# Performance work log

Hardware: AMD Instinct MI355X
Metric: run time of the kernel (lower is better)

Reference implementation:

```python
import jax, jax.numpy as jnp
import numpy as np

E = 64          # num experts
IN = 512        # input_size
OUT = 512       # output_size
N = 131072      # total tokens = sum(expert_size)
CAP = 3072      # static per-expert capacity (>= max expert_size)


def _make_expert_sizes():
    # uneven but deterministic sizes summing to N, all <= CAP
    rng = np.random.default_rng(0)
    sizes = np.full(E, N // E, dtype=np.int32)
    d = rng.integers(0, 513, size=E // 2).astype(np.int32)
    sizes[0::2] += d
    sizes[1::2] -= d
    assert sizes.sum() == N and sizes.max() <= CAP and sizes.min() > 0
    return jnp.asarray(sizes, dtype=jnp.int32)


def setup_inputs() -> dict:
    key = jax.random.key(0)
    k1, k2 = jax.random.split(key)
    inputs = jax.random.normal(k1, (N, IN), dtype=jnp.float32)
    # matches nn.init.uniform_(weight, -1/in, 1/in)
    weight = jax.random.uniform(k2, (E, IN, OUT), dtype=jnp.float32,
                                minval=-1.0 / IN, maxval=1.0 / IN)
    expert_size = _make_expert_sizes()
    return {"inputs": inputs, "expert_size": expert_size, "weight": weight}


def reference(inputs, expert_size, weight):
    # Grouped GEMM: tokens are pre-sorted by expert; segment e is
    # inputs[offset[e]:offset[e]+expert_size[e]] @ weight[e].
    cap_ids = jnp.arange(CAP, dtype=jnp.int32)                # [CAP]
    offsets = jnp.cumsum(expert_size) - expert_size           # [E]
    idx = offsets[:, None] + cap_ids[None, :]                 # [E, CAP]
    valid = cap_ids[None, :] < expert_size[:, None]           # [E, CAP]
    idx = jnp.where(valid, idx, N)                            # invalid -> OOB (dropped)
    # gather tokens into padded per-expert blocks; invalid slots -> 0
    x = jnp.take(inputs, idx, axis=0, mode='fill', fill_value=0.0)  # [E, CAP, IN]
    h = jnp.einsum('eci,eio->eco', x, weight)                 # [E, CAP, OUT]
    out = jnp.zeros((N, OUT), dtype=inputs.dtype)
    out = out.at[idx.reshape(-1)].add(h.reshape(-1, OUT), mode='drop')
    return out
```

## Files before the change

kernel.cpp:

```cpp
#include <hip/hip_runtime.h>
#include <hip/hip_bf16.h>

#define E_NUM 64
#define IN_SZ 512
#define OUT_SZ 512
#define N_TOK 131072
#define CAP 3072

#define BM 128
#define BN 256
#define BK 32
#define THREADS 512
#define RT_MAX 24
#define CT_NUM 2
#define JT 16
#define NWG (E_NUM * RT_MAX * CT_NUM)

typedef __attribute__((ext_vector_type(8))) short short8;
typedef __attribute__((ext_vector_type(4))) float f32x4;

__device__ inline unsigned short f2bf(float f) {
    unsigned int u = __float_as_uint(f);
    unsigned int r = (u + 0x7FFF + ((u >> 16) & 1)) >> 16;
    return (unsigned short)r;
}

#define GLOAD_LDS16(g, l)                                                     \
    __builtin_amdgcn_global_load_lds(                                         \
        (const __attribute__((address_space(1))) void*)(g),                   \
        (__attribute__((address_space(3))) void*)(l), 16, 0, 0)

__global__ void offsets_kernel(const int* __restrict__ sizes, int* __restrict__ offs) {
    int e = threadIdx.x;
    int s = 0;
    for (int i = 0; i < e; ++i) s += sizes[i];
    offs[e] = s;
}

__global__ __launch_bounds__(256) void prep_wt(const float* __restrict__ W,
                                               unsigned short* __restrict__ WT) {
    __shared__ float t[32][33];
    int k0 = blockIdx.x * 32, n0 = blockIdx.y * 32, e = blockIdx.z;
    const float* We = W + (size_t)e * IN_SZ * OUT_SZ;
    int tid = threadIdx.x;
    int r = tid >> 3, c4 = (tid & 7) * 4;
    float4 v = *(const float4*)(We + (size_t)(k0 + r) * OUT_SZ + n0 + c4);
    t[r][c4 + 0] = v.x; t[r][c4 + 1] = v.y; t[r][c4 + 2] = v.z; t[r][c4 + 3] = v.w;
    __syncthreads();
    ushort4 o;
    o.x = f2bf(t[c4 + 0][r]);
    o.y = f2bf(t[c4 + 1][r]);
    o.z = f2bf(t[c4 + 2][r]);
    o.w = f2bf(t[c4 + 3][r]);
    unsigned short* O = WT + (size_t)e * IN_SZ * OUT_SZ + (size_t)(n0 + r) * IN_SZ + k0 + c4;
    *(ushort4*)O = o;
}

__global__ __launch_bounds__(THREADS, 4) void gemm_moe(
    const float* __restrict__ A, const int* __restrict__ sizes,
    const unsigned short* __restrict__ WT, const int* __restrict__ offs,
    float* __restrict__ out)
{
    int b0 = blockIdx.x;
    int wg = (b0 & 7) * (NWG / 8) + (b0 >> 3);
    int ct = wg & (CT_NUM - 1);
    int rt = (wg >> 1) % RT_MAX;
    int e  = wg / (RT_MAX * CT_NUM);

    int size_e = sizes[e];
    int rows0 = rt * BM;
    if (rows0 >= size_e) return;
    int off_e = offs[e];
    int rows_rem = size_e - rows0;
    int maxr = (rows_rem < BM ? rows_rem : BM) - 1;

    __shared__ unsigned short lsA[2][BM * BK];
    __shared__ unsigned short lsB[2][BN * BK];

    int tid = threadIdx.x, l = tid & 63, w = tid >> 6;
    const char* WTe = (const char*)(WT + (size_t)e * IN_SZ * OUT_SZ);
    const float* Abase = A + (size_t)(off_e + rows0) * IN_SZ;

    const float* ap[2];
    int aw[2];
    #pragma unroll
    for (int i = 0; i < 2; ++i) {
        int idx = tid + THREADS * i;
        int row = idx >> 3, c4 = idx & 7;
        int gr = row <= maxr ? row : maxr;
        ap[i] = Abase + (size_t)gr * IN_SZ + c4 * 4;
        aw[i] = row * 64 + ((c4 * 8) ^ (((row >> 1) & 3) << 4));
    }
    const char* gB[2];
    #pragma unroll
    for (int i = 0; i < 2; ++i) {
        int c = w * 2 + i;
        int n = c * 16 + (l >> 2);
        int csrc = ((l & 3) * 16) ^ (((l >> 3) & 3) << 4);
        gB[i] = WTe + (size_t)(ct * BN + n) * (IN_SZ * 2) + csrc;
    }

    float4 ar[2];

    auto loadA = [&](int kt) {
        #pragma unroll
        for (int i = 0; i < 2; ++i)
            ar[i] = *(const float4*)(ap[i] + kt * BK);
    };
    auto writeA = [&](int buf) {
        #pragma unroll
        for (int i = 0; i < 2; ++i) {
            ushort4 pk;
            pk.x = f2bf(ar[i].x); pk.y = f2bf(ar[i].y);
            pk.z = f2bf(ar[i].z); pk.w = f2bf(ar[i].w);
            *(ushort4*)((char*)&lsA[buf][0] + aw[i]) = pk;
        }
    };
    auto stageB = [&](int buf, int kt) {
        #pragma unroll
        for (int i = 0; i < 2; ++i)
            GLOAD_LDS16(gB[i] + kt * 64, &lsB[buf][(w * 2 + i) * 512]);
    };

    int wm = (w >> 2) * 64, wn = (w & 3) * 64;
    int lrow = l & 15;
    int cb = ((l >> 4) * 16) ^ (((l >> 1) & 3) << 4);

    f32x4 acc[4][4] = {};

    loadA(0); stageB(0, 0);
    writeA(0);
    __syncthreads();

    #pragma unroll
    for (int j = 0; j < JT; ++j) {
        int cur = j & 1;
        if (j + 1 < JT) {
            loadA(j + 1);
            stageB(cur ^ 1, j + 1);
        }
        {
            const char* pA = (const char*)&lsA[cur][0];
            const char* pB = (const char*)&lsB[cur][0];
            short8 af[4];
            #pragma unroll
            for (int m = 0; m < 4; ++m)
                af[m] = *(const short8*)(pA + (wm + m * 16 + lrow) * 64 + cb);
            __builtin_amdgcn_s_setprio(1);
            #pragma unroll
            for (int n = 0; n < 4; ++n) {
                short8 bf = *(const short8*)(pB + (wn + n * 16 + lrow) * 64 + cb);
                #pragma unroll
                for (int m = 0; m < 4; ++m)
                    acc[m][n] = __builtin_amdgcn_mfma_f32_16x16x32_bf16(
                        af[m], bf, acc[m][n], 0, 0, 0);
            }
            __builtin_amdgcn_s_setprio(0);
        }
        if (j + 1 < JT)
            writeA(cur ^ 1);
        if (j < JT - 1)
            __syncthreads();
    }

    float* outb = out + (size_t)(off_e + rows0) * OUT_SZ + ct * BN + wn;
    #pragma unroll
    for (int m = 0; m < 4; ++m) {
        #pragma unroll
        for (int j = 0; j < 4; ++j) {
            int rl = wm + m * 16 + (l >> 4) * 4 + j;
            if (rl < rows_rem) {
                float* po = outb + (size_t)rl * OUT_SZ + lrow;
                #pragma unroll
                for (int n = 0; n < 4; ++n)
                    po[n * 16] = acc[m][n][j];
            }
        }
    }
}

extern "C" void kernel_launch(void* const* d_in, const int* in_sizes, int n_in,
                              void* d_out, int out_size, void* d_ws, size_t ws_size,
                              hipStream_t stream) {
    const float* A      = (const float*)d_in[0];
    const int* sizes    = (const int*)d_in[1];
    const float* W      = (const float*)d_in[2];
    float* out          = (float*)d_out;

    unsigned short* WT  = (unsigned short*)d_ws;
    int* offs           = (int*)((char*)d_ws + (size_t)E_NUM * IN_SZ * OUT_SZ * 2);

    offsets_kernel<<<1, E_NUM, 0, stream>>>(sizes, offs);
    prep_wt<<<dim3(IN_SZ / 32, OUT_SZ / 32, E_NUM), 256, 0, stream>>>(W, WT);
    gemm_moe<<<NWG, THREADS, 0, stream>>>(A, sizes, WT, offs, out);
}
```

Baseline: 210.0 us.

## Pre-convert activations to bf16 and stage A tiles via direct global-to-LDS loads

Adds a separate pass that converts the fp32 input activations to bf16 in workspace. The GEMM kernel can then load A tiles with global_load_lds DMA, like the B tiles, instead of register loads plus in-kernel conversion and LDS stores. This removes VGPR staging and conversion work from the main loop. In exchange it adds a full extra read and write of the activation matrix. The old path is kept as a fallback when the workspace is too small.

```diff
diff --git a/kernel.cpp b/kernel.cpp
--- a/kernel.cpp
+++ b/kernel.cpp
@@ -15,6 +15,7 @@
 #define CT_NUM 2
 #define JT 16
 #define NWG (E_NUM * RT_MAX * CT_NUM)
+#define ATOT ((long)N_TOK * IN_SZ)
 
 typedef __attribute__((ext_vector_type(8))) short short8;
 typedef __attribute__((ext_vector_type(4))) float f32x4;
@@ -56,8 +57,24 @@
     *(ushort4*)O = o;
 }
 
-__global__ __launch_bounds__(THREADS, 4) void gemm_moe(
-    const float* __restrict__ A, const int* __restrict__ sizes,
+__global__ __launch_bounds__(256) void prep_a(const float* __restrict__ A,
+                                              unsigned short* __restrict__ Abf) {
+    long i = ((long)blockIdx.x * 256 + threadIdx.x) * 8;
+    long stride = (long)gridDim.x * 256 * 8;
+    for (; i < ATOT; i += stride) {
+        float4 v0 = *(const float4*)(A + i);
+        float4 v1 = *(const float4*)(A + i + 4);
+        short8 o;
+        o[0] = (short)f2bf(v0.x); o[1] = (short)f2bf(v0.y);
+        o[2] = (short)f2bf(v0.z); o[3] = (short)f2bf(v0.w);
+        o[4] = (short)f2bf(v1.x); o[5] = (short)f2bf(v1.y);
+        o[6] = (short)f2bf(v1.z); o[7] = (short)f2bf(v1.w);
+        *(short8*)(Abf + i) = o;
+    }
+}
+
+__global__ __launch_bounds__(THREADS, 4) void gemm_moe_dma(
+    const unsigned short* __restrict__ Abf, const int* __restrict__ sizes,
     const unsigned short* __restrict__ WT, const int* __restrict__ offs,
     float* __restrict__ out)
 {
@@ -78,19 +95,13 @@
     __shared__ unsigned short lsB[2][BN * BK];
 
     int tid = threadIdx.x, l = tid & 63, w = tid >> 6;
+    const char* Ae  = (const char*)(Abf + (size_t)(off_e + rows0) * IN_SZ);
     const char* WTe = (const char*)(WT + (size_t)e * IN_SZ * OUT_SZ);
-    const float* Abase = A + (size_t)(off_e + rows0) * IN_SZ;
-
-    const float* ap[2];
-    int aw[2];
-    #pragma unroll
-    for (int i = 0; i < 2; ++i) {
-        int idx = tid + THREADS * i;
-        int row = idx >> 3, c4 = idx & 7;
-        int gr = row <= maxr ? row : maxr;
-        ap[i] = Abase + (size_t)gr * IN_SZ + c4 * 4;
-        aw[i] = row * 64 + ((c4 * 8) ^ (((row >> 1) & 3) << 4));
-    }
+
+    int arow = w * 16 + (l >> 2);
+    int gar = arow <= maxr ? arow : maxr;
+    const char* gA = Ae + (size_t)gar * (IN_SZ * 2)
+                   + (((l & 3) ^ ((arow >> 1) & 3)) * 16);
     const char* gB[2];
     #pragma unroll
     for (int i = 0; i < 2; ++i) {
@@ -100,21 +111,8 @@
         gB[i] = WTe + (size_t)(ct * BN + n) * (IN_SZ * 2) + csrc;
     }
 
-    float4 ar[2];
-
-    auto loadA = [&](int kt) {
-        #pragma unroll
-        for (int i = 0; i < 2; ++i)
-            ar[i] = *(const float4*)(ap[i] + kt * BK);
-    };
-    auto writeA = [&](int buf) {
-        #pragma unroll
-        for (int i = 0; i < 2; ++i) {
-            ushort4 pk;
-            pk.x = f2bf(ar[i].x); pk.y = f2bf(ar[i].y);
-            pk.z = f2bf(ar[i].z); pk.w = f2bf(ar[i].w);
-            *(ushort4*)((char*)&lsA[buf][0] + aw[i]) = pk;
-        }
+    auto stageA = [&](int buf, int kt) {
+        GLOAD_LDS16(gA + kt * 64, &lsA[buf][w * 512]);
     };
     auto stageB = [&](int buf, int kt) {
         #pragma unroll
@@ -128,15 +126,14 @@
 
     f32x4 acc[4][4] = {};
 
-    loadA(0); stageB(0, 0);
-    writeA(0);
+    stageA(0, 0); stageB(0, 0);
     __syncthreads();
 
     #pragma unroll
     for (int j = 0; j < JT; ++j) {
         int cur = j & 1;
         if (j + 1 < JT) {
-            loadA(j + 1);
+            stageA(cur ^ 1, j + 1);
             stageB(cur ^ 1, j + 1);
         }
         {
@@ -157,8 +154,6 @@
             }
             __builtin_amdgcn_s_setprio(0);
         }
-        if (j + 1 < JT)
-            writeA(cur ^ 1);
         if (j < JT - 1)
             __syncthreads();
     }
@@ -179,6 +174,128 @@
     }
 }
 
+__global__ __launch_bounds__(THREADS, 4) void gemm_moe_reg(
+    const float* __restrict__ A, const int* __restrict__ sizes,
+    const unsigned short* __restrict__ WT, const int* __restrict__ offs,
+    float* __restrict__ out)
+{
+    int b0 = blockIdx.x;
+    int wg = (b0 & 7) * (NWG / 8) + (b0 >> 3);
+    int ct = wg & (CT_NUM - 1);
+    int rt = (wg >> 1) % RT_MAX;
+    int e  = wg / (RT_MAX * CT_NUM);
+
+    int size_e = sizes[e];
+    int rows0 = rt * BM;
+    if (rows0 >= size_e) return;
+    int off_e = offs[e];
+    int rows_rem = size_e - rows0;
+    int maxr = (rows_rem < BM ? rows_rem : BM) - 1;
+
+    __shared__ unsigned short lsA[2][BM * BK];
+    __shared__ unsigned short lsB[2][BN * BK];
+
+    int tid = threadIdx.x, l = tid & 63, w = tid >> 6;
+    const char* WTe = (const char*)(WT + (size_t)e * IN_SZ * OUT_SZ);
+    const float* Abase = A + (size_t)(off_e + rows0) * IN_SZ;
+
+    const float* ap[2];
+    int aw[2];
+    #pragma unroll
+    for (int i = 0; i < 2; ++i) {
+        int idx = tid + THREADS * i;
+        int row = idx >> 3, c4 = idx & 7;
+        int gr = row <= maxr ? row : maxr;
+        ap[i] = Abase + (size_t)gr * IN_SZ + c4 * 4;
+        aw[i] = row * 64 + ((c4 * 8) ^ (((row >> 1) & 3) << 4));
+    }
+    const char* gB[2];
+    #pragma unroll
+    for (int i = 0; i < 2; ++i) {
+        int c = w * 2 + i;
+        int n = c * 16 + (l >> 2);
+        int csrc = ((l & 3) * 16) ^ (((l >> 3) & 3) << 4);
+        gB[i] = WTe + (size_t)(ct * BN + n) * (IN_SZ * 2) + csrc;
+    }
+
+    float4 ar[2];
+    auto loadA = [&](int kt) {
+        #pragma unroll
+        for (int i = 0; i < 2; ++i)
+            ar[i] = *(const float4*)(ap[i] + kt * BK);
+    };
+    auto writeA = [&](int buf) {
+        #pragma unroll
+        for (int i = 0; i < 2; ++i) {
+            ushort4 pk;
+            pk.x = f2bf(ar[i].x); pk.y = f2bf(ar[i].y);
+            pk.z = f2bf(ar[i].z); pk.w = f2bf(ar[i].w);
+            *(ushort4*)((char*)&lsA[buf][0] + aw[i]) = pk;
+        }
+    };
+    auto stageB = [&](int buf, int kt) {
+        #pragma unroll
+        for (int i = 0; i < 2; ++i)
+            GLOAD_LDS16(gB[i] + kt * 64, &lsB[buf][(w * 2 + i) * 512]);
+    };
+
+    int wm = (w >> 2) * 64, wn = (w & 3) * 64;
+    int lrow = l & 15;
+    int cb = ((l >> 4) * 16) ^ (((l >> 1) & 3) << 4);
+
+    f32x4 acc[4][4] = {};
+
+    loadA(0); stageB(0, 0);
+    writeA(0);
+    __syncthreads();
+
+    #pragma unroll
+    for (int j = 0; j < JT; ++j) {
+        int cur = j & 1;
+        if (j + 1 < JT) {
+            loadA(j + 1);
+            stageB(cur ^ 1, j + 1);
+        }
+        {
+            const char* pA = (const char*)&lsA[cur][0];
+            const char* pB = (const char*)&lsB[cur][0];
+            short8 af[4];
+            #pragma unroll
+            for (int m = 0; m < 4; ++m)
+                af[m] = *(const short8*)(pA + (wm + m * 16 + lrow) * 64 + cb);
+            __builtin_amdgcn_s_setprio(1);
+            #pragma unroll
+            for (int n = 0; n < 4; ++n) {
+                short8 bf = *(const short8*)(pB + (wn + n * 16 + lrow) * 64 + cb);
+                #pragma unroll
+                for (int m = 0; m < 4; ++m)
+                    acc[m][n] = __builtin_amdgcn_mfma_f32_16x16x32_bf16(
+                        af[m], bf, acc[m][n], 0, 0, 0);
+            }
+            __builtin_amdgcn_s_setprio(0);
+        }
+        if (j + 1 < JT)
+            writeA(cur ^ 1);
+        if (j < JT - 1)
+            __syncthreads();
+    }
+
+    float* outb = out + (size_t)(off_e + rows0) * OUT_SZ + ct * BN + wn;
+    #pragma unroll
+    for (int m = 0; m < 4; ++m) {
+        #pragma unroll
+        for (int j = 0; j < 4; ++j) {
+            int rl = wm + m * 16 + (l >> 4) * 4 + j;
+            if (rl < rows_rem) {
+                float* po = outb + (size_t)rl * OUT_SZ + lrow;
+                #pragma unroll
+                for (int n = 0; n < 4; ++n)
+                    po[n * 16] = acc[m][n][j];
+            }
+        }
+    }
+}
+
 extern "C" void kernel_launch(void* const* d_in, const int* in_sizes, int n_in,
                               void* d_out, int out_size, void* d_ws, size_t ws_size,
                               hipStream_t stream) {
@@ -187,10 +304,21 @@
     const float* W      = (const float*)d_in[2];
     float* out          = (float*)d_out;
 
+    const size_t WT_BYTES  = (size_t)E_NUM * IN_SZ * OUT_SZ * 2;
+    const size_t ABF_OFF   = WT_BYTES + 65536;
+    const size_t ABF_BYTES = (size_t)ATOT * 2;
+
     unsigned short* WT  = (unsigned short*)d_ws;
-    int* offs           = (int*)((char*)d_ws + (size_t)E_NUM * IN_SZ * OUT_SZ * 2);
+    int* offs           = (int*)((char*)d_ws + WT_BYTES);
 
     offsets_kernel<<<1, E_NUM, 0, stream>>>(sizes, offs);
     prep_wt<<<dim3(IN_SZ / 32, OUT_SZ / 32, E_NUM), 256, 0, stream>>>(W, WT);
-    gemm_moe<<<NWG, THREADS, 0, stream>>>(A, sizes, WT, offs, out);
-}
+
+    if (ws_size >= ABF_OFF + ABF_BYTES) {
+        unsigned short* Abf = (unsigned short*)((char*)d_ws + ABF_OFF);
+        prep_a<<<4096, 256, 0, stream>>>(A, Abf);
+        gemm_moe_dma<<<NWG, THREADS, 0, stream>>>(Abf, sizes, WT, offs, out);
+    } else {
+        gemm_moe_reg<<<NWG, THREADS, 0, stream>>>(A, sizes, WT, offs, out);
+    }
+}
```

New measurement: 243.3 us. +15.9%, slower.

## Enlarge GEMM tile to 256x256x64 with XOR-swizzled LDS and packed bf16 convert

Applied to the files above, without the earlier changes.

Doubles the M tile to 256 rows and the K step to 64, so each warp accumulates an 8x4 grid of MFMA tiles and reuses each loaded B fragment across more A rows. The LDS layout changes to an 8-chunk XOR swizzle for both A and B. The fp32-to-bf16 conversion of A now uses the packed v_cvt_pk_bf16_f32 instruction instead of manual rounding. Occupancy drops to 2 workgroups per CU, the larger accumulator raises register pressure, and row tiles at the tail of each expert carry more padding waste.

```diff
diff --git a/kernel.cpp b/kernel.cpp
--- a/kernel.cpp
+++ b/kernel.cpp
@@ -7,13 +7,13 @@
 #define N_TOK 131072
 #define CAP 3072
 
-#define BM 128
+#define BM 256
 #define BN 256
-#define BK 32
+#define BK 64
 #define THREADS 512
-#define RT_MAX 24
+#define RT_MAX 12
 #define CT_NUM 2
-#define JT 16
+#define JT 8
 #define NWG (E_NUM * RT_MAX * CT_NUM)
 
 typedef __attribute__((ext_vector_type(8))) short short8;
@@ -23,6 +23,12 @@
     unsigned int u = __float_as_uint(f);
     unsigned int r = (u + 0x7FFF + ((u >> 16) & 1)) >> 16;
     return (unsigned short)r;
+}
+
+__device__ inline unsigned int cvtpk(float a, float b) {
+    unsigned int r;
+    asm("v_cvt_pk_bf16_f32 %0, %1, %2" : "=v"(r) : "v"(a), "v"(b));
+    return r;
 }
 
 #define GLOAD_LDS16(g, l)                                                     \
@@ -56,7 +62,7 @@
     *(ushort4*)O = o;
 }
 
-__global__ __launch_bounds__(THREADS, 4) void gemm_moe(
+__global__ __launch_bounds__(THREADS, 2) void gemm_moe(
     const float* __restrict__ A, const int* __restrict__ sizes,
     const unsigned short* __restrict__ WT, const int* __restrict__ offs,
     float* __restrict__ out)
@@ -81,52 +87,61 @@
     const char* WTe = (const char*)(WT + (size_t)e * IN_SZ * OUT_SZ);
     const float* Abase = A + (size_t)(off_e + rows0) * IN_SZ;
 
-    const float* ap[2];
-    int aw[2];
-    #pragma unroll
-    for (int i = 0; i < 2; ++i) {
-        int idx = tid + THREADS * i;
-        int row = idx >> 3, c4 = idx & 7;
+    int aoff[4];
+    #pragma unroll
+    for (int jj = 0; jj < 4; ++jj) {
+        int u = tid + THREADS * jj;
+        int row = u >> 3, s = u & 7;
+        int c = s ^ (row & 7);
         int gr = row <= maxr ? row : maxr;
-        ap[i] = Abase + (size_t)gr * IN_SZ + c4 * 4;
-        aw[i] = row * 64 + ((c4 * 8) ^ (((row >> 1) & 3) << 4));
-    }
-    const char* gB[2];
-    #pragma unroll
-    for (int i = 0; i < 2; ++i) {
-        int c = w * 2 + i;
-        int n = c * 16 + (l >> 2);
-        int csrc = ((l & 3) * 16) ^ (((l >> 3) & 3) << 4);
-        gB[i] = WTe + (size_t)(ct * BN + n) * (IN_SZ * 2) + csrc;
-    }
-
-    float4 ar[2];
+        aoff[jj] = gr * IN_SZ + c * 8;
+    }
+    int boff[4];
+    #pragma unroll
+    for (int i = 0; i < 4; ++i) {
+        int unit = (w * 4 + i) * 64 + l;
+        int row = unit >> 3, s = unit & 7;
+        int c = s ^ (row & 7);
+        boff[i] = (ct * BN + row) * (IN_SZ * 2) + c * 16;
+    }
+
+    f32x4 ar[8];
 
     auto loadA = [&](int kt) {
         #pragma unroll
-        for (int i = 0; i < 2; ++i)
-            ar[i] = *(const float4*)(ap[i] + kt * BK);
+        for (int jj = 0; jj < 4; ++jj) {
+            ar[2 * jj]     = *(const f32x4*)(Abase + aoff[jj] + kt * BK);
+            ar[2 * jj + 1] = *(const f32x4*)(Abase + aoff[jj] + kt * BK + 4);
+        }
     };
     auto writeA = [&](int buf) {
         #pragma unroll
-        for (int i = 0; i < 2; ++i) {
-            ushort4 pk;
-            pk.x = f2bf(ar[i].x); pk.y = f2bf(ar[i].y);
-            pk.z = f2bf(ar[i].z); pk.w = f2bf(ar[i].w);
-            *(ushort4*)((char*)&lsA[buf][0] + aw[i]) = pk;
+        for (int jj = 0; jj < 4; ++jj) {
+            unsigned int p0 = cvtpk(ar[2 * jj][0], ar[2 * jj][1]);
+            unsigned int p1 = cvtpk(ar[2 * jj][2], ar[2 * jj][3]);
+            unsigned int p2 = cvtpk(ar[2 * jj + 1][0], ar[2 * jj + 1][1]);
+            unsigned int p3 = cvtpk(ar[2 * jj + 1][2], ar[2 * jj + 1][3]);
+            uint4 pk = make_uint4(p0, p1, p2, p3);
+            *(uint4*)((char*)&lsA[buf][0] + (tid + THREADS * jj) * 16) = pk;
         }
     };
     auto stageB = [&](int buf, int kt) {
         #pragma unroll
-        for (int i = 0; i < 2; ++i)
-            GLOAD_LDS16(gB[i] + kt * 64, &lsB[buf][(w * 2 + i) * 512]);
+        for (int i = 0; i < 4; ++i)
+            GLOAD_LDS16(WTe + boff[i] + kt * 128, &lsB[buf][(w * 4 + i) * 512]);
     };
 
-    int wm = (w >> 2) * 64, wn = (w & 3) * 64;
-    int lrow = l & 15;
-    int cb = ((l >> 4) * 16) ^ (((l >> 1) & 3) << 4);
-
-    f32x4 acc[4][4] = {};
+    int wm = (w >> 2) * 128, wn = (w & 3) * 64;
+    int lrow = l & 15, kq = l >> 4;
+    int abm[8], bbn[4];
+    #pragma unroll
+    for (int mm = 0; mm < 8; ++mm) abm[mm] = (wm + mm * 16 + lrow) * 128;
+    #pragma unroll
+    for (int nn = 0; nn < 4; ++nn) bbn[nn] = (wn + nn * 16 + lrow) * 128;
+    int sk0 = ((0 * 4 + kq) ^ (lrow & 7)) * 16;
+    int sk1 = ((1 * 4 + kq) ^ (lrow & 7)) * 16;
+
+    f32x4 acc[8][4] = {};
 
     loadA(0); stageB(0, 0);
     writeA(0);
@@ -142,18 +157,22 @@
         {
             const char* pA = (const char*)&lsA[cur][0];
             const char* pB = (const char*)&lsB[cur][0];
-            short8 af[4];
-            #pragma unroll
-            for (int m = 0; m < 4; ++m)
-                af[m] = *(const short8*)(pA + (wm + m * 16 + lrow) * 64 + cb);
             __builtin_amdgcn_s_setprio(1);
             #pragma unroll
-            for (int n = 0; n < 4; ++n) {
-                short8 bf = *(const short8*)(pB + (wn + n * 16 + lrow) * 64 + cb);
+            for (int ks = 0; ks < 2; ++ks) {
+                int sk = ks ? sk1 : sk0;
+                short8 bfr[4];
                 #pragma unroll
-                for (int m = 0; m < 4; ++m)
-                    acc[m][n] = __builtin_amdgcn_mfma_f32_16x16x32_bf16(
-                        af[m], bf, acc[m][n], 0, 0, 0);
+                for (int nn = 0; nn < 4; ++nn)
+                    bfr[nn] = *(const short8*)(pB + bbn[nn] + sk);
+                #pragma unroll
+                for (int mm = 0; mm < 8; ++mm) {
+                    short8 af = *(const short8*)(pA + abm[mm] + sk);
+                    #pragma unroll
+                    for (int nn = 0; nn < 4; ++nn)
+                        acc[mm][nn] = __builtin_amdgcn_mfma_f32_16x16x32_bf16(
+                            af, bfr[nn], acc[mm][nn], 0, 0, 0);
+                }
             }
             __builtin_amdgcn_s_setprio(0);
         }
@@ -165,15 +184,15 @@
 
     float* outb = out + (size_t)(off_e + rows0) * OUT_SZ + ct * BN + wn;
     #pragma unroll
-    for (int m = 0; m < 4; ++m) {
-        #pragma unroll
-        for (int j = 0; j < 4; ++j) {
-            int rl = wm + m * 16 + (l >> 4) * 4 + j;
+    for (int mm = 0; mm < 8; ++mm) {
+        #pragma unroll
+        for (int jj = 0; jj < 4; ++jj) {
+            int rl = wm + mm * 16 + kq * 4 + jj;
             if (rl < rows_rem) {
                 float* po = outb + (size_t)rl * OUT_SZ + lrow;
                 #pragma unroll
-                for (int n = 0; n < 4; ++n)
-                    po[n * 16] = acc[m][n][j];
+                for (int nn = 0; nn < 4; ++nn)
+                    po[nn * 16] = acc[mm][nn][jj];
             }
         }
     }
```

New measurement: 184.5 us (median of 3 runs). 12.2% less time.
